# Kernel tuning notes

Measured on AMD Instinct MI355X. Metric: run time of the kernel, lower is better.

The kernel has to match this reference:

```python
import jax, jax.numpy as jnp
import numpy as np

T, H = 4096, 2048

def _glorot(key, shape):
    return jax.random.uniform(key, shape, minval=-1.0, maxval=1.0) * jnp.sqrt(2.0 / sum(shape))

def setup_inputs() -> dict:
    key = jax.random.key(0)
    kx, ka, kb = jax.random.split(key, 3)
    x = jax.random.normal(kx, (T, H), dtype=jnp.float32)
    a_mat = _glorot(ka, (H,)).astype(jnp.float32)          # |a| < 1 -> stable recurrence
    b_mat = _glorot(kb, (H, H)).astype(jnp.float32)
    return {"x": x, "a_mat": a_mat, "b_mat": b_mat}

def reference(x, a_mat, b_mat):
    # s_t = b_mat.T @ x_t for all t, done as one GEMM: (T,H) @ (H,H)
    s = x @ b_mat  # (T, H)
    def step(h, s_t):
        h = jnp.tanh(a_mat * h + s_t)
        return h, h
    h0 = jnp.zeros_like(a_mat)
    _, h_seq = jax.lax.scan(step, h0, s)
    return h_seq  # (T, H)
```

## Files before the change

kernel.cpp:

```cpp
#include <hip/hip_runtime.h>
#include <stdint.h>
#include <stddef.h>

#define Tdim 4096
#define Hdim 2048

typedef short short8 __attribute__((ext_vector_type(8)));
typedef float floatx4 __attribute__((ext_vector_type(4)));

__device__ __forceinline__ unsigned short f2bf(float f) {
  uint32_t u = __float_as_uint(f);
  u += 0x7fffu + ((u >> 16) & 1u);
  return (unsigned short)(u >> 16);
}

__device__ __forceinline__ void load_lds16(const void* g, void* l) {
  __builtin_amdgcn_global_load_lds(
      (__attribute__((address_space(1))) unsigned int*)(uintptr_t)g,
      (__attribute__((address_space(3))) unsigned int*)l,
      16, 0, 0);
}

__device__ __forceinline__ float tanh_fast(float z) {
  float e = __expf(z + z);
  return 1.0f - __fdividef(2.0f, e + 1.0f);
}

__device__ __forceinline__ short8 lds_read8(const unsigned short* p) {
  return *(const short8*)__builtin_assume_aligned(p, 16);
}

__global__ __launch_bounds__(256) void cvt_kernel(const float* __restrict__ x,
                                                  const float* __restrict__ b,
                                                  unsigned short* __restrict__ xbf,
                                                  unsigned short* __restrict__ bt) {
  __shared__ unsigned short tile[64 * 65];
  const int t = threadIdx.x;
  if (blockIdx.x < 4096) {
    size_t i = ((size_t)blockIdx.x * 256 + t) * 8;
    float4 f0 = *(const float4*)(x + i);
    float4 f1 = *(const float4*)(x + i + 4);
    union { unsigned short u[8]; uint4 v; } o;
    o.u[0] = f2bf(f0.x); o.u[1] = f2bf(f0.y); o.u[2] = f2bf(f0.z); o.u[3] = f2bf(f0.w);
    o.u[4] = f2bf(f1.x); o.u[5] = f2bf(f1.y); o.u[6] = f2bf(f1.z); o.u[7] = f2bf(f1.w);
    *(uint4*)(xbf + i) = o.v;
    return;
  }
  const int tb = blockIdx.x - 4096;
  const int bj = tb & 31;
  const int bi = tb >> 5;
  {
    const int r0 = t >> 4, c4 = (t & 15) * 4;
#pragma unroll
    for (int p = 0; p < 4; ++p) {
      int r = r0 + p * 16;
      float4 v = *(const float4*)(b + (size_t)(bi * 64 + r) * Hdim + bj * 64 + c4);
      tile[r * 65 + c4 + 0] = f2bf(v.x);
      tile[r * 65 + c4 + 1] = f2bf(v.y);
      tile[r * 65 + c4 + 2] = f2bf(v.z);
      tile[r * 65 + c4 + 3] = f2bf(v.w);
    }
  }
  __syncthreads();
  {
    const int n = t >> 2, kq = (t & 3) * 16;
    union { unsigned short u[16]; uint4 v[2]; } o;
#pragma unroll
    for (int q = 0; q < 16; ++q) o.u[q] = tile[(kq + q) * 65 + n];
    uint4* dst = (uint4*)(bt + (size_t)(bj * 64 + n) * Hdim + bi * 64 + kq);
    dst[0] = o.v[0];
    dst[1] = o.v[1];
  }
}

#define BARM() asm volatile("s_barrier" ::: "memory")
#define WAITV(N) asm volatile("s_waitcnt vmcnt(" #N ")" ::: "memory")
#define WAITL0() asm volatile("s_waitcnt lgkmcnt(0)" ::: "memory")

__global__ __launch_bounds__(512, 2) void gemm_scan_kernel(const unsigned short* __restrict__ A,
                                                           const unsigned short* __restrict__ Bt,
                                                           const float* __restrict__ a_mat,
                                                           float* __restrict__ out) {
  __shared__ alignas(16) union SM {
    struct {
      unsigned short sA[3][256 * 64];
      unsigned short sB[3][128 * 64];
      unsigned short sAw[3][8 * 64];
    } st;
    float s_tile[264 * 129];
  } sm;

  const int tid = threadIdx.x;
  const int b0 = blockIdx.x;
  const int nid = (b0 & 7) * 32 + (b0 >> 3);
  const int bm = nid >> 4;
  const int bn = nid & 15;
  const int wave = tid >> 6, lane = tid & 63;
  const int wm = (wave >> 1) * 64, wn = (wave & 1) * 64;
  const int l15 = lane & 15, quad = lane >> 4;
  const int l7 = l15 & 7;

  const int swz = ((tid & 7) ^ ((tid >> 3) & 7)) * 8;
  const unsigned short* aSrc = A + ((size_t)(bm * 256 + (tid >> 3)) * Hdim + swz);
  const unsigned short* bSrc = Bt + ((size_t)(bn * 128 + (tid >> 3)) * Hdim + swz);
  const int tw0 = (bm > 0) ? bm * 256 - 8 : 0;
  const int wswz = ((lane & 7) ^ ((lane >> 3) & 7)) * 8;
  const unsigned short* wSrc = A + ((size_t)(tw0 + (lane >> 3)) * Hdim + wswz);

  floatx4 acc[4][4] = {};
  floatx4 accw[4] = {};

  const int c0 = (quad ^ l7) * 8;
  const int c1 = c0 ^ 32;
  int rA[4], rB[4];
#pragma unroll
  for (int i = 0; i < 4; ++i) rA[i] = (wm + i * 16 + l15) * 64;
#pragma unroll
  for (int j = 0; j < 4; ++j) rB[j] = (wn + j * 16 + l15) * 64;

  auto stage_p0 = [&](int nb, int k0) {
    unsigned short* aDst = &sm.st.sA[nb][tid * 8];
    load_lds16(aSrc + k0, aDst);
    load_lds16(aSrc + (size_t)64 * Hdim + k0, aDst + 4096);
    load_lds16(bSrc + k0, &sm.st.sB[nb][tid * 8]);
  };
  auto stage_p1 = [&](int nb, int k0) {
    unsigned short* aDst = &sm.st.sA[nb][tid * 8];
    load_lds16(aSrc + (size_t)128 * Hdim + k0, aDst + 8192);
    load_lds16(aSrc + (size_t)192 * Hdim + k0, aDst + 12288);
    load_lds16(bSrc + (size_t)64 * Hdim + k0, &sm.st.sB[nb][tid * 8 + 4096]);
    if (wave == 7) load_lds16(wSrc + k0, &sm.st.sAw[nb][lane * 8]);
  };

  stage_p0(0, 0);  stage_p1(0, 0);
  stage_p0(1, 64); stage_p1(1, 64);
  if (wave == 7) { WAITV(7); } else { WAITV(6); }
  BARM();

  int buf = 0;
  for (int t = 0; t < 32; ++t) {
    const int nb = (buf >= 1) ? buf - 1 : 2;
    const bool pf = (t < 30);
    const int k2 = (t + 2) * 64;
    const unsigned short* sAb = sm.st.sA[buf];
    const unsigned short* sBb = sm.st.sB[buf];
    const unsigned short* sWb = sm.st.sAw[buf];

    short8 av[4], bv[4], aw = {};

#pragma unroll
    for (int i = 0; i < 4; ++i) av[i] = lds_read8(sAb + rA[i] + c0);
#pragma unroll
    for (int j = 0; j < 4; ++j) bv[j] = lds_read8(sBb + rB[j] + c0);
    if (wave < 2) aw = lds_read8(sWb + l7 * 64 + c0);
    if (pf) stage_p0(nb, k2);
    BARM();
    WAITL0();
    __builtin_amdgcn_sched_barrier(0);
    __builtin_amdgcn_s_setprio(1);
#pragma unroll
    for (int i = 0; i < 4; ++i)
#pragma unroll
      for (int j = 0; j < 4; ++j)
        acc[i][j] = __builtin_amdgcn_mfma_f32_16x16x32_bf16(av[i], bv[j], acc[i][j], 0, 0, 0);
    if (wave < 2) {
#pragma unroll
      for (int j = 0; j < 4; ++j)
        accw[j] = __builtin_amdgcn_mfma_f32_16x16x32_bf16(aw, bv[j], accw[j], 0, 0, 0);
    }
    __builtin_amdgcn_s_setprio(0);
    BARM();

#pragma unroll
    for (int i = 0; i < 4; ++i) av[i] = lds_read8(sAb + rA[i] + c1);
#pragma unroll
    for (int j = 0; j < 4; ++j) bv[j] = lds_read8(sBb + rB[j] + c1);
    if (wave < 2) aw = lds_read8(sWb + l7 * 64 + c1);
    if (pf) stage_p1(nb, k2);
    BARM();
    WAITL0();
    __builtin_amdgcn_sched_barrier(0);
    __builtin_amdgcn_s_setprio(1);
#pragma unroll
    for (int i = 0; i < 4; ++i)
#pragma unroll
      for (int j = 0; j < 4; ++j)
        acc[i][j] = __builtin_amdgcn_mfma_f32_16x16x32_bf16(av[i], bv[j], acc[i][j], 0, 0, 0);
    if (wave < 2) {
#pragma unroll
      for (int j = 0; j < 4; ++j)
        accw[j] = __builtin_amdgcn_mfma_f32_16x16x32_bf16(aw, bv[j], accw[j], 0, 0, 0);
    }
    __builtin_amdgcn_s_setprio(0);
    if (t < 30) {
      if (wave == 7) { WAITV(7); } else { WAITV(6); }
    } else if (t == 30) {
      WAITV(0);
    }
    BARM();
    buf = (buf == 2) ? 0 : buf + 1;
  }
  __syncthreads();

  if (wave < 2 && quad < 2) {
#pragma unroll
    for (int j = 0; j < 4; ++j)
#pragma unroll
      for (int r = 0; r < 4; ++r)
        sm.s_tile[(quad * 4 + r) * 129 + wn + j * 16 + l15] = accw[j][r];
  }
#pragma unroll
  for (int i = 0; i < 4; ++i)
#pragma unroll
    for (int j = 0; j < 4; ++j)
#pragma unroll
      for (int r = 0; r < 4; ++r)
        sm.s_tile[(8 + wm + i * 16 + quad * 4 + r) * 129 + wn + j * 16 + l15] = acc[i][j][r];
  __syncthreads();

  const int col = tid & 127;
  const int chunk = tid >> 7;
  const float aj = a_mat[bn * 128 + col];
  float h = 0.0f;
  const int row0 = 8 + chunk * 64;
  if (!(bm == 0 && chunk == 0)) {
#pragma unroll
    for (int r = row0 - 8; r < row0; ++r)
      h = tanh_fast(fmaf(aj, h, sm.s_tile[r * 129 + col]));
  }
  const size_t gbase = (size_t)(bm * 256 + chunk * 64) * Hdim + bn * 128 + col;
#pragma unroll 4
  for (int r2 = 0; r2 < 64; ++r2) {
    h = tanh_fast(fmaf(aj, h, sm.s_tile[(row0 + r2) * 129 + col]));
    out[gbase + (size_t)r2 * Hdim] = h;
  }
}

extern "C" void kernel_launch(void* const* d_in, const int* in_sizes, int n_in,
                              void* d_out, int out_size, void* d_ws, size_t ws_size,
                              hipStream_t stream) {
  const float* x = (const float*)d_in[0];
  const float* a = (const float*)d_in[1];
  const float* b = (const float*)d_in[2];
  float* out = (float*)d_out;

  unsigned short* ws = (unsigned short*)d_ws;
  unsigned short* xbf = ws;
  unsigned short* btb = xbf + (size_t)Tdim * Hdim;

  hipLaunchKernelGGL(cvt_kernel, dim3(4096 + (Hdim / 64) * (Hdim / 64)), dim3(256), 0, stream,
                     x, b, xbf, btb);
  hipLaunchKernelGGL(gemm_scan_kernel, dim3((Tdim / 256) * (Hdim / 128)), dim3(512), 0, stream,
                     xbf, btb, a, out);
}
```

Baseline: 142.2 us.

## Split GEMM main loop into four finer-grained load/compute phases

Each 32-wide k-half of the main loop is split into two phases that each read half the B fragments and issue a subset of the next-stage global-to-LDS loads. This spreads the loads and LDS reads more evenly between MFMA bursts. It also drops the XCD-aware block remapping in favour of a plain 2D grid, which may change L2 locality across chiplets. The extra barriers per iteration add synchronisation overhead, and the vmcnt wait counts stay the same even though the loads are now issued in a different order.

Measured after the change: 142.7 us. About the same (+0.4%).

```diff
diff --git a/kernel.cpp b/kernel.cpp
--- a/kernel.cpp
+++ b/kernel.cpp
@@ -29,6 +29,20 @@
 __device__ __forceinline__ short8 lds_read8(const unsigned short* p) {
   return *(const short8*)__builtin_assume_aligned(p, 16);
 }
+
+#define BARM() asm volatile("s_barrier" ::: "memory")
+#define WAITV(N) asm volatile("s_waitcnt vmcnt(" #N ")" ::: "memory")
+#define LGKM0()                                                        \
+  do {                                                                 \
+    asm volatile("s_waitcnt lgkmcnt(0)" ::: "memory");                 \
+    __builtin_amdgcn_sched_barrier(0);                                 \
+  } while (0)
+
+#define SYNC_DRAIN()                                                   \
+  do {                                                                 \
+    asm volatile("s_waitcnt vmcnt(0) lgkmcnt(0)" ::: "memory");        \
+    __syncthreads();                                                   \
+  } while (0)
 
 __global__ __launch_bounds__(256) void cvt_kernel(const float* __restrict__ x,
                                                   const float* __restrict__ b,
@@ -73,10 +87,6 @@
   }
 }
 
-#define BARM() asm volatile("s_barrier" ::: "memory")
-#define WAITV(N) asm volatile("s_waitcnt vmcnt(" #N ")" ::: "memory")
-#define WAITL0() asm volatile("s_waitcnt lgkmcnt(0)" ::: "memory")
-
 __global__ __launch_bounds__(512, 2) void gemm_scan_kernel(const unsigned short* __restrict__ A,
                                                            const unsigned short* __restrict__ Bt,
                                                            const float* __restrict__ a_mat,
@@ -91,12 +101,10 @@
   } sm;
 
   const int tid = threadIdx.x;
-  const int b0 = blockIdx.x;
-  const int nid = (b0 & 7) * 32 + (b0 >> 3);
-  const int bm = nid >> 4;
-  const int bn = nid & 15;
+  const int bm = blockIdx.x, bn = blockIdx.y;
   const int wave = tid >> 6, lane = tid & 63;
-  const int wm = (wave >> 1) * 64, wn = (wave & 1) * 64;
+  const int wm = (wave >> 1) * 64;
+  const int wn = (wave & 1) * 64;
   const int l15 = lane & 15, quad = lane >> 4;
   const int l7 = l15 & 7;
 
@@ -117,23 +125,22 @@
   for (int i = 0; i < 4; ++i) rA[i] = (wm + i * 16 + l15) * 64;
 #pragma unroll
   for (int j = 0; j < 4; ++j) rB[j] = (wn + j * 16 + l15) * 64;
-
-  auto stage_p0 = [&](int nb, int k0) {
+  const int rW = l7 * 64;
+
+  auto stage_full = [&](int nb, int k0) {
     unsigned short* aDst = &sm.st.sA[nb][tid * 8];
-    load_lds16(aSrc + k0, aDst);
-    load_lds16(aSrc + (size_t)64 * Hdim + k0, aDst + 4096);
-    load_lds16(bSrc + k0, &sm.st.sB[nb][tid * 8]);
-  };
-  auto stage_p1 = [&](int nb, int k0) {
-    unsigned short* aDst = &sm.st.sA[nb][tid * 8];
-    load_lds16(aSrc + (size_t)128 * Hdim + k0, aDst + 8192);
-    load_lds16(aSrc + (size_t)192 * Hdim + k0, aDst + 12288);
-    load_lds16(bSrc + (size_t)64 * Hdim + k0, &sm.st.sB[nb][tid * 8 + 4096]);
+    unsigned short* bDst = &sm.st.sB[nb][tid * 8];
+#pragma unroll
+    for (int c = 0; c < 4; ++c)
+      load_lds16(aSrc + (size_t)c * 64 * Hdim + k0, aDst + c * 4096);
+#pragma unroll
+    for (int c = 0; c < 2; ++c)
+      load_lds16(bSrc + (size_t)c * 64 * Hdim + k0, bDst + c * 4096);
     if (wave == 7) load_lds16(wSrc + k0, &sm.st.sAw[nb][lane * 8]);
   };
 
-  stage_p0(0, 0);  stage_p1(0, 0);
-  stage_p0(1, 64); stage_p1(1, 64);
+  stage_full(0, 0);
+  stage_full(1, 64);
   if (wave == 7) { WAITV(7); } else { WAITV(6); }
   BARM();
 
@@ -145,25 +152,46 @@
     const unsigned short* sAb = sm.st.sA[buf];
     const unsigned short* sBb = sm.st.sB[buf];
     const unsigned short* sWb = sm.st.sAw[buf];
+    unsigned short* aDst = &sm.st.sA[nb][tid * 8];
+    unsigned short* bDst = &sm.st.sB[nb][tid * 8];
 
     short8 av[4], bv[4], aw = {};
 
 #pragma unroll
     for (int i = 0; i < 4; ++i) av[i] = lds_read8(sAb + rA[i] + c0);
-#pragma unroll
-    for (int j = 0; j < 4; ++j) bv[j] = lds_read8(sBb + rB[j] + c0);
-    if (wave < 2) aw = lds_read8(sWb + l7 * 64 + c0);
-    if (pf) stage_p0(nb, k2);
-    BARM();
-    WAITL0();
-    __builtin_amdgcn_sched_barrier(0);
-    __builtin_amdgcn_s_setprio(1);
-#pragma unroll
-    for (int i = 0; i < 4; ++i)
-#pragma unroll
-      for (int j = 0; j < 4; ++j)
-        acc[i][j] = __builtin_amdgcn_mfma_f32_16x16x32_bf16(av[i], bv[j], acc[i][j], 0, 0, 0);
-    if (wave < 2) {
+    bv[0] = lds_read8(sBb + rB[0] + c0);
+    bv[1] = lds_read8(sBb + rB[1] + c0);
+    if (pf) {
+      load_lds16(aSrc + k2, aDst);
+      load_lds16(aSrc + (size_t)64 * Hdim + k2, aDst + 4096);
+    }
+    BARM();
+    LGKM0();
+    __builtin_amdgcn_s_setprio(1);
+#pragma unroll
+    for (int i = 0; i < 4; ++i) {
+      acc[i][0] = __builtin_amdgcn_mfma_f32_16x16x32_bf16(av[i], bv[0], acc[i][0], 0, 0, 0);
+      acc[i][1] = __builtin_amdgcn_mfma_f32_16x16x32_bf16(av[i], bv[1], acc[i][1], 0, 0, 0);
+    }
+    __builtin_amdgcn_s_setprio(0);
+    BARM();
+
+    bv[2] = lds_read8(sBb + rB[2] + c0);
+    bv[3] = lds_read8(sBb + rB[3] + c0);
+    if (wm == 0) aw = lds_read8(sWb + rW + c0);
+    if (pf) {
+      load_lds16(aSrc + (size_t)128 * Hdim + k2, aDst + 8192);
+      load_lds16(aSrc + (size_t)192 * Hdim + k2, aDst + 12288);
+    }
+    BARM();
+    LGKM0();
+    __builtin_amdgcn_s_setprio(1);
+#pragma unroll
+    for (int i = 0; i < 4; ++i) {
+      acc[i][2] = __builtin_amdgcn_mfma_f32_16x16x32_bf16(av[i], bv[2], acc[i][2], 0, 0, 0);
+      acc[i][3] = __builtin_amdgcn_mfma_f32_16x16x32_bf16(av[i], bv[3], acc[i][3], 0, 0, 0);
+    }
+    if (wm == 0) {
 #pragma unroll
       for (int j = 0; j < 4; ++j)
         accw[j] = __builtin_amdgcn_mfma_f32_16x16x32_bf16(aw, bv[j], accw[j], 0, 0, 0);
@@ -173,20 +201,36 @@
 
 #pragma unroll
     for (int i = 0; i < 4; ++i) av[i] = lds_read8(sAb + rA[i] + c1);
-#pragma unroll
-    for (int j = 0; j < 4; ++j) bv[j] = lds_read8(sBb + rB[j] + c1);
-    if (wave < 2) aw = lds_read8(sWb + l7 * 64 + c1);
-    if (pf) stage_p1(nb, k2);
-    BARM();
-    WAITL0();
-    __builtin_amdgcn_sched_barrier(0);
-    __builtin_amdgcn_s_setprio(1);
-#pragma unroll
-    for (int i = 0; i < 4; ++i)
-#pragma unroll
-      for (int j = 0; j < 4; ++j)
-        acc[i][j] = __builtin_amdgcn_mfma_f32_16x16x32_bf16(av[i], bv[j], acc[i][j], 0, 0, 0);
-    if (wave < 2) {
+    bv[0] = lds_read8(sBb + rB[0] + c1);
+    bv[1] = lds_read8(sBb + rB[1] + c1);
+    if (pf) {
+      load_lds16(bSrc + k2, bDst);
+      load_lds16(bSrc + (size_t)64 * Hdim + k2, bDst + 4096);
+    }
+    BARM();
+    LGKM0();
+    __builtin_amdgcn_s_setprio(1);
+#pragma unroll
+    for (int i = 0; i < 4; ++i) {
+      acc[i][0] = __builtin_amdgcn_mfma_f32_16x16x32_bf16(av[i], bv[0], acc[i][0], 0, 0, 0);
+      acc[i][1] = __builtin_amdgcn_mfma_f32_16x16x32_bf16(av[i], bv[1], acc[i][1], 0, 0, 0);
+    }
+    __builtin_amdgcn_s_setprio(0);
+    BARM();
+
+    bv[2] = lds_read8(sBb + rB[2] + c1);
+    bv[3] = lds_read8(sBb + rB[3] + c1);
+    if (wm == 0) aw = lds_read8(sWb + rW + c1);
+    if (pf && wave == 7) load_lds16(wSrc + k2, &sm.st.sAw[nb][lane * 8]);
+    BARM();
+    LGKM0();
+    __builtin_amdgcn_s_setprio(1);
+#pragma unroll
+    for (int i = 0; i < 4; ++i) {
+      acc[i][2] = __builtin_amdgcn_mfma_f32_16x16x32_bf16(av[i], bv[2], acc[i][2], 0, 0, 0);
+      acc[i][3] = __builtin_amdgcn_mfma_f32_16x16x32_bf16(av[i], bv[3], acc[i][3], 0, 0, 0);
+    }
+    if (wm == 0) {
 #pragma unroll
       for (int j = 0; j < 4; ++j)
         accw[j] = __builtin_amdgcn_mfma_f32_16x16x32_bf16(aw, bv[j], accw[j], 0, 0, 0);
@@ -200,9 +244,9 @@
     BARM();
     buf = (buf == 2) ? 0 : buf + 1;
   }
-  __syncthreads();
-
-  if (wave < 2 && quad < 2) {
+  SYNC_DRAIN();
+
+  if (wm == 0 && quad < 2) {
 #pragma unroll
     for (int j = 0; j < 4; ++j)
 #pragma unroll
@@ -216,7 +260,7 @@
 #pragma unroll
       for (int r = 0; r < 4; ++r)
         sm.s_tile[(8 + wm + i * 16 + quad * 4 + r) * 129 + wn + j * 16 + l15] = acc[i][j][r];
-  __syncthreads();
+  SYNC_DRAIN();
 
   const int col = tid & 127;
   const int chunk = tid >> 7;
@@ -250,6 +294,6 @@
 
   hipLaunchKernelGGL(cvt_kernel, dim3(4096 + (Hdim / 64) * (Hdim / 64)), dim3(256), 0, stream,
                      x, b, xbf, btb);
-  hipLaunchKernelGGL(gemm_scan_kernel, dim3((Tdim / 256) * (Hdim / 128)), dim3(512), 0, stream,
+  hipLaunchKernelGGL(gemm_scan_kernel, dim3(Tdim / 256, Hdim / 128), dim3(512), 0, stream,
                      xbf, btb, a, out);
 }
```
